# Optimization experiments

Hardware: AMD Instinct MI355X
Metric: run time of the kernel (lower is better)

The kernel has to match this reference:

```python
import jax, jax.numpy as jnp
import numpy as np

N = 50000      # nodes
E = 800000     # edges (avg degree 16)
D = 64         # emb_dim
L = 5          # num_layer
X_DIM = 92     # atom feature dim (hardwired in module)
EA_DIM = 50    # edge feature dim (edge_dim=50)
BN_EPS = 1e-5


def setup_inputs() -> dict:
    key = jax.random.key(0)
    ks = jax.random.split(key, 12)
    s = 0.05
    return {
        "x": jax.random.normal(ks[0], (N, X_DIM), jnp.float32),
        "edge_index": jax.random.randint(ks[1], (2, E), 0, N, dtype=jnp.int64),
        "edge_attr": jax.random.normal(ks[2], (E, EA_DIM), jnp.float32),
        # atom encoder: Linear(92, D)
        "atom_W": jax.random.normal(ks[3], (X_DIM, D), jnp.float32) * s,
        "atom_b": jnp.zeros((D,), jnp.float32),
        # per-layer GINEConv edge lin: Linear(50, D)
        "edge_W": jax.random.normal(ks[4], (L, EA_DIM, D), jnp.float32) * s,
        "edge_b": jnp.zeros((L, D), jnp.float32),
        # per-layer GIN MLP: Linear(D,D) -> ReLU -> Linear(D,D)
        "mlp_W1": jax.random.normal(ks[5], (L, D, D), jnp.float32) * s,
        "mlp_b1": jnp.zeros((L, D), jnp.float32),
        "mlp_W2": jax.random.normal(ks[6], (L, D, D), jnp.float32) * s,
        "mlp_b2": jnp.zeros((L, D), jnp.float32),
        # learnable eps (train_eps=True, init 0)
        "eps": jnp.zeros((L,), jnp.float32),
        # batch norm affine params
        "bn_gamma": jnp.ones((L, D), jnp.float32),
        "bn_beta": jnp.zeros((L, D), jnp.float32),
    }


def reference(x, edge_index, edge_attr, atom_W, atom_b, edge_W, edge_b,
              mlp_W1, mlp_b1, mlp_W2, mlp_b2, eps, bn_gamma, bn_beta):
    # edge_index[0] = src (message source), edge_index[1] = dst (aggregation target)
    # (adj = SparseTensor(row=ei[0], col=ei[1]); conv uses adj.t() -> aggregate at ei[1])
    src, dst = edge_index[0], edge_index[1]
    h = x @ atom_W + atom_b  # [N, D] atom encoder
    for l in range(L):
        # GINEConv message: relu(x_j + lin(edge_attr)), summed at destination
        m = jax.nn.relu(h[src] + edge_attr @ edge_W[l] + edge_b[l])  # [E, D]
        agg = jax.ops.segment_sum(m, dst, num_segments=N)             # [N, D]
        z = (1.0 + eps[l]) * h + agg
        z = jax.nn.relu(z @ mlp_W1[l] + mlp_b1[l]) @ mlp_W2[l] + mlp_b2[l]
        # BatchNorm1d (batch statistics over nodes)
        mu = jnp.mean(z, axis=0)
        var = jnp.var(z, axis=0)
        z = bn_gamma[l] * (z - mu) * jax.lax.rsqrt(var + BN_EPS) + bn_beta[l]
        # relu on all but last layer (dropout inactive in eval); residual=False
        h = z if l == L - 1 else jax.nn.relu(z)
    return h  # JK='last'
```

## Files before the change

kernel.cpp:

```cpp
#include <hip/hip_runtime.h>


#define NN 50000
#define NE 800000
#define D 64
#define NL 5
#define XD 92
#define EAD 50
#define BN_EPS 1e-5f
#define NBLK ((NN + 255) / 256)

__global__ void k_prep(const float* __restrict__ atomW, const float* __restrict__ W1,
                       const float* __restrict__ W2, float* __restrict__ atomWt,
                       float* __restrict__ W1t, float* __restrict__ W2t) {
  int tid = blockIdx.x * blockDim.x + threadIdx.x;
  int nt = gridDim.x * blockDim.x;
  for (int i = tid; i < XD * D; i += nt) {
    int k = i / D, d = i % D;
    atomWt[d * XD + k] = atomW[i];
  }
  for (int i = tid; i < NL * D * D; i += nt) {
    int l = i / (D * D), r = i % (D * D);
    int k = r / D, d = r % D;
    W1t[(l * D + d) * D + k] = W1[i];
    W2t[(l * D + d) * D + k] = W2[i];
  }
}

__global__ __launch_bounds__(256) void k_atom(const float* __restrict__ x,
    const float* __restrict__ Wt, const float* __restrict__ b,
    float* __restrict__ h) {
  int n = blockIdx.x * blockDim.x + threadIdx.x;
  if (n >= NN) return;
  const float* xp = x + (size_t)n * XD;
  float xr[XD];
#pragma unroll
  for (int k = 0; k < XD; k += 4) {
    float4 v = *reinterpret_cast<const float4*>(xp + k);
    xr[k] = v.x; xr[k + 1] = v.y; xr[k + 2] = v.z; xr[k + 3] = v.w;
  }
  float hr[D];
#pragma unroll
  for (int d = 0; d < D; ++d) {
    const float* wr = Wt + d * XD;
    float a0 = 0.f, a1 = 0.f, a2 = 0.f, a3 = 0.f;
#pragma unroll
    for (int k = 0; k < XD; k += 4) {
      a0 = fmaf(xr[k + 0], wr[k + 0], a0);
      a1 = fmaf(xr[k + 1], wr[k + 1], a1);
      a2 = fmaf(xr[k + 2], wr[k + 2], a2);
      a3 = fmaf(xr[k + 3], wr[k + 3], a3);
    }
    hr[d] = (a0 + a1) + (a2 + a3) + b[d];
  }
  float* hp = h + (size_t)n * D;
#pragma unroll
  for (int d = 0; d < D; d += 4)
    *reinterpret_cast<float4*>(hp + d) = make_float4(hr[d], hr[d+1], hr[d+2], hr[d+3]);
}

__global__ __launch_bounds__(256) void k_deg(const int* __restrict__ ei,
                                             int* __restrict__ deg) {
  int e = blockIdx.x * blockDim.x + threadIdx.x;
  if (e < NE) atomicAdd(&deg[ei[NE + e]], 1);
}

__global__ __launch_bounds__(256) void k_scan_a(const int* __restrict__ deg,
    int* __restrict__ lps, int* __restrict__ bsum) {
  __shared__ int s[256];
  int t = threadIdx.x;
  int i = blockIdx.x * 256 + t;
  int v = (i < NN) ? deg[i] : 0;
  s[t] = v;
  __syncthreads();
#pragma unroll
  for (int off = 1; off < 256; off <<= 1) {
    int xv = (t >= off) ? s[t - off] : 0;
    __syncthreads();
    s[t] += xv;
    __syncthreads();
  }
  if (i < NN) lps[i] = s[t] - v;
  if (t == 255) bsum[blockIdx.x] = s[255];
}

__global__ __launch_bounds__(256) void k_scan_b(const int* __restrict__ bsum,
                                                int* __restrict__ bpre) {
  __shared__ int s[256];
  int t = threadIdx.x;
  int v = (t < NBLK) ? bsum[t] : 0;
  s[t] = v;
  __syncthreads();
#pragma unroll
  for (int off = 1; off < 256; off <<= 1) {
    int xv = (t >= off) ? s[t - off] : 0;
    __syncthreads();
    s[t] += xv;
    __syncthreads();
  }
  bpre[t] = s[t] - v;
}

__global__ __launch_bounds__(256) void k_fill(const int* __restrict__ lps,
    const int* __restrict__ bpre, int* __restrict__ rowptr,
    int* __restrict__ cursor) {
  int i = blockIdx.x * blockDim.x + threadIdx.x;
  if (i < NN) {
    int v = lps[i] + bpre[i >> 8];
    rowptr[i] = v;
    cursor[i] = v;
  }
  if (i == 0) rowptr[NN] = NE;
}

__global__ __launch_bounds__(256) void k_scatter(const int* __restrict__ ei,
    int* __restrict__ cursor, int* __restrict__ esrc, int* __restrict__ eidl) {
  int e = blockIdx.x * blockDim.x + threadIdx.x;
  if (e >= NE) return;
  int dst = ei[NE + e];
  int p = atomicAdd(&cursor[dst], 1);
  esrc[p] = ei[e];
  eidl[p] = e;
}

__global__ __launch_bounds__(256) void k_aggr(const float* __restrict__ h,
    const float* __restrict__ ea, const float* __restrict__ eW,
    const float* __restrict__ eb, const int* __restrict__ rowptr,
    const int* __restrict__ esrc, const int* __restrict__ eidl,
    const float* __restrict__ eps, int layer, float* __restrict__ z) {
  int lane = threadIdx.x & 63;
  int wid = __builtin_amdgcn_readfirstlane(blockIdx.x * 4 + (threadIdx.x >> 6));
  int nw = gridDim.x * 4;
  const float* Wl = eW + (size_t)layer * EAD * D;
  float wc[EAD];
#pragma unroll
  for (int k = 0; k < EAD; ++k) wc[k] = Wl[k * D + lane];
  float bd = eb[layer * D + lane];
  float ope = 1.f + eps[layer];
  for (int n = wid; n < NN; n += nw) {
    int beg = __builtin_amdgcn_readfirstlane(rowptr[n]);
    int end = __builtin_amdgcn_readfirstlane(rowptr[n + 1]);
    float acc = 0.f;
    for (int idx = beg; idx < end; ++idx) {
      int e   = __builtin_amdgcn_readfirstlane(eidl[idx]);
      int src = __builtin_amdgcn_readfirstlane(esrc[idx]);
      const float2* ep2 = reinterpret_cast<const float2*>(ea + (size_t)e * EAD);
      float a0 = 0.f, a1 = 0.f, a2 = 0.f, a3 = 0.f;
#pragma unroll
      for (int k2 = 0; k2 < 24; k2 += 2) {
        float2 p0 = ep2[k2];
        float2 p1 = ep2[k2 + 1];
        a0 = fmaf(p0.x, wc[2 * k2 + 0], a0);
        a1 = fmaf(p0.y, wc[2 * k2 + 1], a1);
        a2 = fmaf(p1.x, wc[2 * k2 + 2], a2);
        a3 = fmaf(p1.y, wc[2 * k2 + 3], a3);
      }
      float2 pt = ep2[24];
      a0 = fmaf(pt.x, wc[48], a0);
      a1 = fmaf(pt.y, wc[49], a1);
      float lin = (a0 + a1) + (a2 + a3) + bd;
      acc += fmaxf(h[(size_t)src * D + lane] + lin, 0.f);
    }
    z[(size_t)n * D + lane] = fmaf(ope, h[(size_t)n * D + lane], acc);
  }
}

__global__ __launch_bounds__(256) void k_mlp(const float* __restrict__ W1t,
    const float* __restrict__ b1, const float* __restrict__ W2t,
    const float* __restrict__ b2, int layer, float* __restrict__ z) {
  int n = blockIdx.x * blockDim.x + threadIdx.x;
  if (n >= NN) return;
  float* zp = z + (size_t)n * D;
  float zr[D];
#pragma unroll
  for (int k = 0; k < D; k += 4) {
    float4 v = *reinterpret_cast<const float4*>(zp + k);
    zr[k] = v.x; zr[k+1] = v.y; zr[k+2] = v.z; zr[k+3] = v.w;
  }
  const float* W1l = W1t + (size_t)layer * D * D;
  const float* b1l = b1 + layer * D;
  float y[D];
#pragma unroll
  for (int d = 0; d < D; ++d) {
    const float* wr = W1l + d * D;
    float a0 = 0.f, a1 = 0.f, a2 = 0.f, a3 = 0.f;
#pragma unroll
    for (int k = 0; k < D; k += 4) {
      a0 = fmaf(zr[k + 0], wr[k + 0], a0);
      a1 = fmaf(zr[k + 1], wr[k + 1], a1);
      a2 = fmaf(zr[k + 2], wr[k + 2], a2);
      a3 = fmaf(zr[k + 3], wr[k + 3], a3);
    }
    y[d] = fmaxf((a0 + a1) + (a2 + a3) + b1l[d], 0.f);
  }
  const float* W2l = W2t + (size_t)layer * D * D;
  const float* b2l = b2 + layer * D;
#pragma unroll
  for (int d = 0; d < D; ++d) {
    const float* wr = W2l + d * D;
    float a0 = 0.f, a1 = 0.f, a2 = 0.f, a3 = 0.f;
#pragma unroll
    for (int k = 0; k < D; k += 4) {
      a0 = fmaf(y[k + 0], wr[k + 0], a0);
      a1 = fmaf(y[k + 1], wr[k + 1], a1);
      a2 = fmaf(y[k + 2], wr[k + 2], a2);
      a3 = fmaf(y[k + 3], wr[k + 3], a3);
    }
    zr[d] = (a0 + a1) + (a2 + a3) + b2l[d];
  }
#pragma unroll
  for (int d = 0; d < D; d += 4)
    *reinterpret_cast<float4*>(zp + d) = make_float4(zr[d], zr[d+1], zr[d+2], zr[d+3]);
}

__global__ __launch_bounds__(256) void k_stats(const float* __restrict__ t,
                                               float* __restrict__ stats) {
  int lane = threadIdx.x & 63;
  int w = threadIdx.x >> 6;
  int gw = blockIdx.x * 4 + w;
  int nw = gridDim.x * 4;
  float s = 0.f, q = 0.f;
  for (int n = gw; n < NN; n += nw) {
    float v = t[(size_t)n * D + lane];
    s += v;
    q = fmaf(v, v, q);
  }
  __shared__ float ls[8][64];
  ls[w][lane] = s;
  ls[4 + w][lane] = q;
  __syncthreads();
  if (threadIdx.x < D) {
    float S = ls[0][lane] + ls[1][lane] + ls[2][lane] + ls[3][lane];
    float Q = ls[4][lane] + ls[5][lane] + ls[6][lane] + ls[7][lane];
    unsafeAtomicAdd(&stats[lane], S);
    unsafeAtomicAdd(&stats[D + lane], Q);
  }
}

__global__ __launch_bounds__(256) void k_apply(const float* __restrict__ t,
    const float* __restrict__ stats, const float* __restrict__ gamma,
    const float* __restrict__ beta, int layer, int last, float* __restrict__ o) {
  const float inv = 1.f / (float)NN;
  int i = blockIdx.x * blockDim.x + threadIdx.x;
  int nt = gridDim.x * blockDim.x;
  for (; i < NN * D / 4; i += nt) {
    int d0 = (i & 15) * 4;
    float4 v = reinterpret_cast<const float4*>(t)[i];
    float vv[4] = {v.x, v.y, v.z, v.w};
    float r[4];
#pragma unroll
    for (int c = 0; c < 4; ++c) {
      int d = d0 + c;
      float mu = stats[d] * inv;
      float var = fmaf(-mu, mu, stats[D + d] * inv);
      float sc = gamma[layer * D + d] / sqrtf(var + BN_EPS);
      float val = fmaf(vv[c] - mu, sc, beta[layer * D + d]);
      r[c] = last ? val : fmaxf(val, 0.f);
    }
    reinterpret_cast<float4*>(o)[i] = make_float4(r[0], r[1], r[2], r[3]);
  }
}

extern "C" void kernel_launch(void* const* d_in, const int* in_sizes, int n_in,
                              void* d_out, int out_size, void* d_ws, size_t ws_size,
                              hipStream_t stream) {
  const float* x     = (const float*)d_in[0];
  const int*   ei    = (const int*)d_in[1];
  const float* ea    = (const float*)d_in[2];
  const float* atomW = (const float*)d_in[3];
  const float* atomB = (const float*)d_in[4];
  const float* eW    = (const float*)d_in[5];
  const float* eb    = (const float*)d_in[6];
  const float* W1    = (const float*)d_in[7];
  const float* b1    = (const float*)d_in[8];
  const float* W2    = (const float*)d_in[9];
  const float* b2    = (const float*)d_in[10];
  const float* eps   = (const float*)d_in[11];
  const float* gamma = (const float*)d_in[12];
  const float* beta  = (const float*)d_in[13];
  float* out = (float*)d_out;

  char* ws = (char*)d_ws;
  float* h      = (float*)ws;
  float* z      = h + (size_t)NN * D;
  float* stats  = z + (size_t)NN * D;
  float* atomWt = stats + 2 * D;
  float* W1t    = atomWt + D * XD;
  float* W2t    = W1t + NL * D * D;
  int*   deg    = (int*)(W2t + NL * D * D);
  int*   lps    = deg + NN;
  int*   rowptr = lps + NN;
  int*   cursor = rowptr + NN + 1;
  int*   bsum   = cursor + NN;
  int*   bpre   = bsum + 256;
  int*   esrc   = bpre + 256;
  int*   eidl   = esrc + NE;

  k_prep<<<64, 256, 0, stream>>>(atomW, W1, W2, atomWt, W1t, W2t);
  k_atom<<<(NN + 255) / 256, 256, 0, stream>>>(x, atomWt, atomB, h);

  hipMemsetAsync(deg, 0, (size_t)NN * 4, stream);
  k_deg<<<(NE + 255) / 256, 256, 0, stream>>>(ei, deg);
  k_scan_a<<<NBLK, 256, 0, stream>>>(deg, lps, bsum);
  k_scan_b<<<1, 256, 0, stream>>>(bsum, bpre);
  k_fill<<<NBLK, 256, 0, stream>>>(lps, bpre, rowptr, cursor);
  k_scatter<<<(NE + 255) / 256, 256, 0, stream>>>(ei, cursor, esrc, eidl);

  for (int l = 0; l < NL; ++l) {
    hipMemsetAsync(stats, 0, 2 * D * 4, stream);
    k_aggr<<<3125, 256, 0, stream>>>(h, ea, eW, eb, rowptr, esrc, eidl, eps, l, z);
    k_mlp<<<(NN + 255) / 256, 256, 0, stream>>>(W1t, b1, W2t, b2, l, z);
    k_stats<<<512, 256, 0, stream>>>(z, stats);
    float* ho = (l == NL - 1) ? out : h;
    k_apply<<<1024, 256, 0, stream>>>(z, stats, gamma, beta, l, (l == NL - 1) ? 1 : 0, ho);
  }
}
```

Measured before the change: 2.054 ms.

## Switch aggregation to edge-tiled segmented atomics and stage weights in LDS

New measurement: 5.527 ms. 2.69x slower.

```diff
diff --git a/kernel.cpp b/kernel.cpp
--- a/kernel.cpp
+++ b/kernel.cpp
@@ -9,6 +9,7 @@
 #define EAD 50
 #define BN_EPS 1e-5f
 #define NBLK ((NN + 255) / 256)
+#define TILE_E 128
 
 __global__ void k_prep(const float* __restrict__ atomW, const float* __restrict__ W1,
                        const float* __restrict__ W2, float* __restrict__ atomWt,
@@ -30,6 +31,9 @@
 __global__ __launch_bounds__(256) void k_atom(const float* __restrict__ x,
     const float* __restrict__ Wt, const float* __restrict__ b,
     float* __restrict__ h) {
+  __shared__ float sw[D * XD];
+  for (int i = threadIdx.x; i < D * XD; i += 256) sw[i] = Wt[i];
+  __syncthreads();
   int n = blockIdx.x * blockDim.x + threadIdx.x;
   if (n >= NN) return;
   const float* xp = x + (size_t)n * XD;
@@ -42,14 +46,15 @@
   float hr[D];
 #pragma unroll
   for (int d = 0; d < D; ++d) {
-    const float* wr = Wt + d * XD;
+    const float4* wr = reinterpret_cast<const float4*>(&sw[d * XD]);
     float a0 = 0.f, a1 = 0.f, a2 = 0.f, a3 = 0.f;
 #pragma unroll
-    for (int k = 0; k < XD; k += 4) {
-      a0 = fmaf(xr[k + 0], wr[k + 0], a0);
-      a1 = fmaf(xr[k + 1], wr[k + 1], a1);
-      a2 = fmaf(xr[k + 2], wr[k + 2], a2);
-      a3 = fmaf(xr[k + 3], wr[k + 3], a3);
+    for (int q = 0; q < XD / 4; ++q) {
+      float4 w = wr[q];
+      a0 = fmaf(xr[4 * q + 0], w.x, a0);
+      a1 = fmaf(xr[4 * q + 1], w.y, a1);
+      a2 = fmaf(xr[4 * q + 2], w.z, a2);
+      a3 = fmaf(xr[4 * q + 3], w.w, a3);
     }
     hr[d] = (a0 + a1) + (a2 + a3) + b[d];
   }
@@ -114,103 +119,143 @@
 }
 
 __global__ __launch_bounds__(256) void k_scatter(const int* __restrict__ ei,
-    int* __restrict__ cursor, int* __restrict__ esrc, int* __restrict__ eidl) {
+    int* __restrict__ cursor, int* __restrict__ esrc, int* __restrict__ eidl,
+    int* __restrict__ dstp) {
   int e = blockIdx.x * blockDim.x + threadIdx.x;
   if (e >= NE) return;
   int dst = ei[NE + e];
   int p = atomicAdd(&cursor[dst], 1);
   esrc[p] = ei[e];
   eidl[p] = e;
-}
-
-__global__ __launch_bounds__(256) void k_aggr(const float* __restrict__ h,
+  dstp[p] = dst;
+}
+
+__global__ __launch_bounds__(256) void k_edge(const float* __restrict__ h,
     const float* __restrict__ ea, const float* __restrict__ eW,
-    const float* __restrict__ eb, const int* __restrict__ rowptr,
-    const int* __restrict__ esrc, const int* __restrict__ eidl,
-    const float* __restrict__ eps, int layer, float* __restrict__ z) {
-  int lane = threadIdx.x & 63;
-  int wid = __builtin_amdgcn_readfirstlane(blockIdx.x * 4 + (threadIdx.x >> 6));
-  int nw = gridDim.x * 4;
+    const float* __restrict__ eb, const int* __restrict__ esrc,
+    const int* __restrict__ eidl, const int* __restrict__ dstp,
+    int layer, float* __restrict__ agg) {
+  __shared__ float2 sea2[TILE_E * 26];
+  __shared__ int s_src[TILE_E], s_dst[TILE_E], s_eid[TILE_E];
+  int tid = threadIdx.x;
+  int lane = tid & 63;
+  int slot0 = blockIdx.x * TILE_E;
+
   const float* Wl = eW + (size_t)layer * EAD * D;
   float wc[EAD];
 #pragma unroll
   for (int k = 0; k < EAD; ++k) wc[k] = Wl[k * D + lane];
   float bd = eb[layer * D + lane];
-  float ope = 1.f + eps[layer];
-  for (int n = wid; n < NN; n += nw) {
-    int beg = __builtin_amdgcn_readfirstlane(rowptr[n]);
-    int end = __builtin_amdgcn_readfirstlane(rowptr[n + 1]);
-    float acc = 0.f;
-    for (int idx = beg; idx < end; ++idx) {
-      int e   = __builtin_amdgcn_readfirstlane(eidl[idx]);
-      int src = __builtin_amdgcn_readfirstlane(esrc[idx]);
-      const float2* ep2 = reinterpret_cast<const float2*>(ea + (size_t)e * EAD);
-      float a0 = 0.f, a1 = 0.f, a2 = 0.f, a3 = 0.f;
-#pragma unroll
-      for (int k2 = 0; k2 < 24; k2 += 2) {
-        float2 p0 = ep2[k2];
-        float2 p1 = ep2[k2 + 1];
-        a0 = fmaf(p0.x, wc[2 * k2 + 0], a0);
-        a1 = fmaf(p0.y, wc[2 * k2 + 1], a1);
-        a2 = fmaf(p1.x, wc[2 * k2 + 2], a2);
-        a3 = fmaf(p1.y, wc[2 * k2 + 3], a3);
-      }
-      float2 pt = ep2[24];
-      a0 = fmaf(pt.x, wc[48], a0);
-      a1 = fmaf(pt.y, wc[49], a1);
-      float lin = (a0 + a1) + (a2 + a3) + bd;
-      acc += fmaxf(h[(size_t)src * D + lane] + lin, 0.f);
-    }
-    z[(size_t)n * D + lane] = fmaf(ope, h[(size_t)n * D + lane], acc);
-  }
-}
-
-__global__ __launch_bounds__(256) void k_mlp(const float* __restrict__ W1t,
-    const float* __restrict__ b1, const float* __restrict__ W2t,
-    const float* __restrict__ b2, int layer, float* __restrict__ z) {
+
+  if (tid < TILE_E) {
+    s_eid[tid] = eidl[slot0 + tid];
+    s_src[tid] = esrc[slot0 + tid];
+    s_dst[tid] = dstp[slot0 + tid];
+  }
+  __syncthreads();
+  for (int i = tid; i < TILE_E * 25; i += 256) {
+    int el = i / 25, k2 = i % 25;
+    sea2[el * 26 + k2] =
+        *reinterpret_cast<const float2*>(ea + (size_t)s_eid[el] * EAD + 2 * k2);
+  }
+  __syncthreads();
+
+  int e0 = (tid >> 6) * 32;
+  int cur = s_dst[e0];
+  float acc = 0.f;
+#pragma unroll 2
+  for (int j = 0; j < 32; ++j) {
+    int el = e0 + j;
+    int dst = s_dst[el];
+    int src = s_src[el];
+    if (dst != cur) {
+      unsafeAtomicAdd(&agg[(size_t)cur * D + lane], acc);
+      acc = 0.f;
+      cur = dst;
+    }
+    const float4* er = reinterpret_cast<const float4*>(&sea2[el * 26]);
+    float a0 = 0.f, a1 = 0.f, a2 = 0.f, a3 = 0.f;
+#pragma unroll
+    for (int q = 0; q < 12; ++q) {
+      float4 v = er[q];
+      a0 = fmaf(v.x, wc[4 * q + 0], a0);
+      a1 = fmaf(v.y, wc[4 * q + 1], a1);
+      a2 = fmaf(v.z, wc[4 * q + 2], a2);
+      a3 = fmaf(v.w, wc[4 * q + 3], a3);
+    }
+    float2 tl = sea2[el * 26 + 24];
+    a0 = fmaf(tl.x, wc[48], a0);
+    a1 = fmaf(tl.y, wc[49], a1);
+    float lin = (a0 + a1) + (a2 + a3) + bd;
+    acc += fmaxf(h[(size_t)src * D + lane] + lin, 0.f);
+  }
+  unsafeAtomicAdd(&agg[(size_t)cur * D + lane], acc);
+}
+
+__global__ __launch_bounds__(256) void k_mlp(const float* __restrict__ h,
+    const float* __restrict__ W1t, const float* __restrict__ b1,
+    const float* __restrict__ W2t, const float* __restrict__ b2,
+    const float* __restrict__ eps, int layer, float* __restrict__ agg) {
+  __shared__ float w1[D * D];
+  __shared__ float w2[D * D];
+  {
+    const float* W1l = W1t + (size_t)layer * D * D;
+    const float* W2l = W2t + (size_t)layer * D * D;
+    for (int i = threadIdx.x; i < D * D; i += 256) {
+      w1[i] = W1l[i];
+      w2[i] = W2l[i];
+    }
+  }
+  __syncthreads();
   int n = blockIdx.x * blockDim.x + threadIdx.x;
   if (n >= NN) return;
-  float* zp = z + (size_t)n * D;
+  float ope = 1.f + eps[layer];
+  const float* hp = h + (size_t)n * D;
+  float* ap = (float*)(agg + (size_t)n * D);
   float zr[D];
 #pragma unroll
   for (int k = 0; k < D; k += 4) {
-    float4 v = *reinterpret_cast<const float4*>(zp + k);
-    zr[k] = v.x; zr[k+1] = v.y; zr[k+2] = v.z; zr[k+3] = v.w;
-  }
-  const float* W1l = W1t + (size_t)layer * D * D;
+    float4 hv = *reinterpret_cast<const float4*>(hp + k);
+    float4 av = *reinterpret_cast<const float4*>(ap + k);
+    zr[k]   = fmaf(ope, hv.x, av.x);
+    zr[k+1] = fmaf(ope, hv.y, av.y);
+    zr[k+2] = fmaf(ope, hv.z, av.z);
+    zr[k+3] = fmaf(ope, hv.w, av.w);
+  }
   const float* b1l = b1 + layer * D;
   float y[D];
 #pragma unroll
   for (int d = 0; d < D; ++d) {
-    const float* wr = W1l + d * D;
+    const float4* wr = reinterpret_cast<const float4*>(&w1[d * D]);
     float a0 = 0.f, a1 = 0.f, a2 = 0.f, a3 = 0.f;
 #pragma unroll
-    for (int k = 0; k < D; k += 4) {
-      a0 = fmaf(zr[k + 0], wr[k + 0], a0);
-      a1 = fmaf(zr[k + 1], wr[k + 1], a1);
-      a2 = fmaf(zr[k + 2], wr[k + 2], a2);
-      a3 = fmaf(zr[k + 3], wr[k + 3], a3);
+    for (int q = 0; q < D / 4; ++q) {
+      float4 w = wr[q];
+      a0 = fmaf(zr[4 * q + 0], w.x, a0);
+      a1 = fmaf(zr[4 * q + 1], w.y, a1);
+      a2 = fmaf(zr[4 * q + 2], w.z, a2);
+      a3 = fmaf(zr[4 * q + 3], w.w, a3);
     }
     y[d] = fmaxf((a0 + a1) + (a2 + a3) + b1l[d], 0.f);
   }
-  const float* W2l = W2t + (size_t)layer * D * D;
   const float* b2l = b2 + layer * D;
 #pragma unroll
   for (int d = 0; d < D; ++d) {
-    const float* wr = W2l + d * D;
+    const float4* wr = reinterpret_cast<const float4*>(&w2[d * D]);
     float a0 = 0.f, a1 = 0.f, a2 = 0.f, a3 = 0.f;
 #pragma unroll
-    for (int k = 0; k < D; k += 4) {
-      a0 = fmaf(y[k + 0], wr[k + 0], a0);
-      a1 = fmaf(y[k + 1], wr[k + 1], a1);
-      a2 = fmaf(y[k + 2], wr[k + 2], a2);
-      a3 = fmaf(y[k + 3], wr[k + 3], a3);
+    for (int q = 0; q < D / 4; ++q) {
+      float4 w = wr[q];
+      a0 = fmaf(y[4 * q + 0], w.x, a0);
+      a1 = fmaf(y[4 * q + 1], w.y, a1);
+      a2 = fmaf(y[4 * q + 2], w.z, a2);
+      a3 = fmaf(y[4 * q + 3], w.w, a3);
     }
     zr[d] = (a0 + a1) + (a2 + a3) + b2l[d];
   }
 #pragma unroll
   for (int d = 0; d < D; d += 4)
-    *reinterpret_cast<float4*>(zp + d) = make_float4(zr[d], zr[d+1], zr[d+2], zr[d+3]);
+    *reinterpret_cast<float4*>(ap + d) = make_float4(zr[d], zr[d+1], zr[d+2], zr[d+3]);
 }
 
 __global__ __launch_bounds__(256) void k_stats(const float* __restrict__ t,
@@ -282,8 +327,8 @@
 
   char* ws = (char*)d_ws;
   float* h      = (float*)ws;
-  float* z      = h + (size_t)NN * D;
-  float* stats  = z + (size_t)NN * D;
+  float* agg    = h + (size_t)NN * D;
+  float* stats  = agg + (size_t)NN * D;
   float* atomWt = stats + 2 * D;
   float* W1t    = atomWt + D * XD;
   float* W2t    = W1t + NL * D * D;
@@ -295,6 +340,7 @@
   int*   bpre   = bsum + 256;
   int*   esrc   = bpre + 256;
   int*   eidl   = esrc + NE;
+  int*   dstp   = eidl + NE;
 
   k_prep<<<64, 256, 0, stream>>>(atomW, W1, W2, atomWt, W1t, W2t);
   k_atom<<<(NN + 255) / 256, 256, 0, stream>>>(x, atomWt, atomB, h);
@@ -304,14 +350,14 @@
   k_scan_a<<<NBLK, 256, 0, stream>>>(deg, lps, bsum);
   k_scan_b<<<1, 256, 0, stream>>>(bsum, bpre);
   k_fill<<<NBLK, 256, 0, stream>>>(lps, bpre, rowptr, cursor);
-  k_scatter<<<(NE + 255) / 256, 256, 0, stream>>>(ei, cursor, esrc, eidl);
+  k_scatter<<<(NE + 255) / 256, 256, 0, stream>>>(ei, cursor, esrc, eidl, dstp);
 
   for (int l = 0; l < NL; ++l) {
-    hipMemsetAsync(stats, 0, 2 * D * 4, stream);
-    k_aggr<<<3125, 256, 0, stream>>>(h, ea, eW, eb, rowptr, esrc, eidl, eps, l, z);
-    k_mlp<<<(NN + 255) / 256, 256, 0, stream>>>(W1t, b1, W2t, b2, l, z);
-    k_stats<<<512, 256, 0, stream>>>(z, stats);
+    hipMemsetAsync(agg, 0, ((size_t)NN * D + 2 * D) * 4, stream);
+    k_edge<<<NE / TILE_E, 256, 0, stream>>>(h, ea, eW, eb, esrc, eidl, dstp, l, agg);
+    k_mlp<<<NBLK, 256, 0, stream>>>(h, W1t, b1, W2t, b2, eps, l, agg);
+    k_stats<<<512, 256, 0, stream>>>(agg, stats);
     float* ho = (l == NL - 1) ? out : h;
-    k_apply<<<1024, 256, 0, stream>>>(z, stats, gamma, beta, l, (l == NL - 1) ? 1 : 0, ho);
-  }
-}
+    k_apply<<<1024, 256, 0, stream>>>(agg, stats, gamma, beta, l, (l == NL - 1) ? 1 : 0, ho);
+  }
+}
```

## Replace per-node aggregation with edge-tiled message kernel and segmented atomic reduction

Applied to the files above, without the earlier changes.

Result: slower. 2.221 ms (+8.1%).

```diff
diff --git a/kernel.cpp b/kernel.cpp
--- a/kernel.cpp
+++ b/kernel.cpp
@@ -9,10 +9,12 @@
 #define EAD 50
 #define BN_EPS 1e-5f
 #define NBLK ((NN + 255) / 256)
+#define TILE_E 256
 
 __global__ void k_prep(const float* __restrict__ atomW, const float* __restrict__ W1,
-                       const float* __restrict__ W2, float* __restrict__ atomWt,
-                       float* __restrict__ W1t, float* __restrict__ W2t) {
+                       const float* __restrict__ W2, const float* __restrict__ eW,
+                       float* __restrict__ atomWt, float* __restrict__ W1t,
+                       float* __restrict__ W2t, float* __restrict__ eWt) {
   int tid = blockIdx.x * blockDim.x + threadIdx.x;
   int nt = gridDim.x * blockDim.x;
   for (int i = tid; i < XD * D; i += nt) {
@@ -24,6 +26,11 @@
     int k = r / D, d = r % D;
     W1t[(l * D + d) * D + k] = W1[i];
     W2t[(l * D + d) * D + k] = W2[i];
+  }
+  for (int i = tid; i < NL * EAD * D; i += nt) {
+    int l = i / (EAD * D), r = i % (EAD * D);
+    int k = r / D, d = r % D;
+    eWt[(l * D + d) * EAD + k] = eW[i];
   }
 }
 
@@ -114,68 +121,104 @@
 }
 
 __global__ __launch_bounds__(256) void k_scatter(const int* __restrict__ ei,
-    int* __restrict__ cursor, int* __restrict__ esrc, int* __restrict__ eidl) {
+    int* __restrict__ cursor, int* __restrict__ esrc, int* __restrict__ eidl,
+    int* __restrict__ dstp) {
   int e = blockIdx.x * blockDim.x + threadIdx.x;
   if (e >= NE) return;
   int dst = ei[NE + e];
   int p = atomicAdd(&cursor[dst], 1);
   esrc[p] = ei[e];
   eidl[p] = e;
-}
-
-__global__ __launch_bounds__(256) void k_aggr(const float* __restrict__ h,
-    const float* __restrict__ ea, const float* __restrict__ eW,
-    const float* __restrict__ eb, const int* __restrict__ rowptr,
-    const int* __restrict__ esrc, const int* __restrict__ eidl,
-    const float* __restrict__ eps, int layer, float* __restrict__ z) {
-  int lane = threadIdx.x & 63;
-  int wid = __builtin_amdgcn_readfirstlane(blockIdx.x * 4 + (threadIdx.x >> 6));
-  int nw = gridDim.x * 4;
-  const float* Wl = eW + (size_t)layer * EAD * D;
-  float wc[EAD];
-#pragma unroll
-  for (int k = 0; k < EAD; ++k) wc[k] = Wl[k * D + lane];
-  float bd = eb[layer * D + lane];
-  float ope = 1.f + eps[layer];
-  for (int n = wid; n < NN; n += nw) {
-    int beg = __builtin_amdgcn_readfirstlane(rowptr[n]);
-    int end = __builtin_amdgcn_readfirstlane(rowptr[n + 1]);
+  dstp[p] = dst;
+}
+
+__global__ __launch_bounds__(256) void k_edge(const float* __restrict__ h,
+    const float* __restrict__ ea, const float* __restrict__ eWt,
+    const float* __restrict__ eb, const int* __restrict__ esrc,
+    const int* __restrict__ eidl, const int* __restrict__ dstp,
+    int layer, float* __restrict__ agg) {
+  __shared__ float msg[4][64 * 33];
+  int tid = threadIdx.x;
+  int lane = tid & 63;
+  int w = tid >> 6;
+  int slot = blockIdx.x * TILE_E + w * 64 + lane;
+
+  int eid  = eidl[slot];
+  int vsrc = esrc[slot];
+  int vdst = dstp[slot];
+
+  const float* ep = ea + (size_t)eid * EAD;
+  float4 ear[13];
+#pragma unroll
+  for (int q = 0; q < 12; ++q)
+    ear[q] = *reinterpret_cast<const float4*>(ep + 4 * q);
+  {
+    float2 t2 = *reinterpret_cast<const float2*>(ep + 48);
+    ear[12] = make_float4(t2.x, t2.y, 0.f, 0.f);
+  }
+
+  const float* Wl = eWt + (size_t)layer * D * EAD;
+  const float* bl = eb + (size_t)layer * D;
+  float* mw = msg[w];
+  int half = lane >> 5;
+  int l31 = lane & 31;
+
+#pragma unroll
+  for (int c = 0; c < 2; ++c) {
+#pragma unroll 2
+    for (int dc = 0; dc < 32; ++dc) {
+      int d = c * 32 + dc;
+      const float* wr = Wl + d * EAD;
+      float a0 = 0.f, a1 = 0.f, a2 = 0.f, a3 = 0.f;
+#pragma unroll
+      for (int q = 0; q < 12; ++q) {
+        a0 = fmaf(ear[q].x, wr[4 * q + 0], a0);
+        a1 = fmaf(ear[q].y, wr[4 * q + 1], a1);
+        a2 = fmaf(ear[q].z, wr[4 * q + 2], a2);
+        a3 = fmaf(ear[q].w, wr[4 * q + 3], a3);
+      }
+      a0 = fmaf(ear[12].x, wr[48], a0);
+      a1 = fmaf(ear[12].y, wr[49], a1);
+      mw[lane * 33 + dc] = (a0 + a1) + (a2 + a3) + bl[d];
+    }
     float acc = 0.f;
-    for (int idx = beg; idx < end; ++idx) {
-      int e   = __builtin_amdgcn_readfirstlane(eidl[idx]);
-      int src = __builtin_amdgcn_readfirstlane(esrc[idx]);
-      const float2* ep2 = reinterpret_cast<const float2*>(ea + (size_t)e * EAD);
-      float a0 = 0.f, a1 = 0.f, a2 = 0.f, a3 = 0.f;
-#pragma unroll
-      for (int k2 = 0; k2 < 24; k2 += 2) {
-        float2 p0 = ep2[k2];
-        float2 p1 = ep2[k2 + 1];
-        a0 = fmaf(p0.x, wc[2 * k2 + 0], a0);
-        a1 = fmaf(p0.y, wc[2 * k2 + 1], a1);
-        a2 = fmaf(p1.x, wc[2 * k2 + 2], a2);
-        a3 = fmaf(p1.y, wc[2 * k2 + 3], a3);
+    int cur = __shfl(vdst, half);
+#pragma unroll 4
+    for (int i = 0; i < 32; ++i) {
+      int e = 2 * i + half;
+      int dste = __shfl(vdst, e);
+      int srce = __shfl(vsrc, e);
+      if (dste != cur) {
+        unsafeAtomicAdd(&agg[(size_t)cur * D + c * 32 + l31], acc);
+        acc = 0.f;
+        cur = dste;
       }
-      float2 pt = ep2[24];
-      a0 = fmaf(pt.x, wc[48], a0);
-      a1 = fmaf(pt.y, wc[49], a1);
-      float lin = (a0 + a1) + (a2 + a3) + bd;
-      acc += fmaxf(h[(size_t)src * D + lane] + lin, 0.f);
-    }
-    z[(size_t)n * D + lane] = fmaf(ope, h[(size_t)n * D + lane], acc);
-  }
-}
-
-__global__ __launch_bounds__(256) void k_mlp(const float* __restrict__ W1t,
-    const float* __restrict__ b1, const float* __restrict__ W2t,
-    const float* __restrict__ b2, int layer, float* __restrict__ z) {
+      float lin = mw[e * 33 + l31];
+      float hv = h[(size_t)srce * D + c * 32 + l31];
+      acc += fmaxf(hv + lin, 0.f);
+    }
+    unsafeAtomicAdd(&agg[(size_t)cur * D + c * 32 + l31], acc);
+  }
+}
+
+__global__ __launch_bounds__(256) void k_mlp(const float* __restrict__ h,
+    const float* __restrict__ W1t, const float* __restrict__ b1,
+    const float* __restrict__ W2t, const float* __restrict__ b2,
+    const float* __restrict__ eps, int layer, float* __restrict__ agg) {
   int n = blockIdx.x * blockDim.x + threadIdx.x;
   if (n >= NN) return;
-  float* zp = z + (size_t)n * D;
+  float ope = 1.f + eps[layer];
+  const float* hp = h + (size_t)n * D;
+  float* ap = agg + (size_t)n * D;
   float zr[D];
 #pragma unroll
   for (int k = 0; k < D; k += 4) {
-    float4 v = *reinterpret_cast<const float4*>(zp + k);
-    zr[k] = v.x; zr[k+1] = v.y; zr[k+2] = v.z; zr[k+3] = v.w;
+    float4 hv = *reinterpret_cast<const float4*>(hp + k);
+    float4 av = *reinterpret_cast<const float4*>(ap + k);
+    zr[k]   = fmaf(ope, hv.x, av.x);
+    zr[k+1] = fmaf(ope, hv.y, av.y);
+    zr[k+2] = fmaf(ope, hv.z, av.z);
+    zr[k+3] = fmaf(ope, hv.w, av.w);
   }
   const float* W1l = W1t + (size_t)layer * D * D;
   const float* b1l = b1 + layer * D;
@@ -210,7 +253,7 @@
   }
 #pragma unroll
   for (int d = 0; d < D; d += 4)
-    *reinterpret_cast<float4*>(zp + d) = make_float4(zr[d], zr[d+1], zr[d+2], zr[d+3]);
+    *reinterpret_cast<float4*>(ap + d) = make_float4(zr[d], zr[d+1], zr[d+2], zr[d+3]);
 }
 
 __global__ __launch_bounds__(256) void k_stats(const float* __restrict__ t,
@@ -282,12 +325,13 @@
 
   char* ws = (char*)d_ws;
   float* h      = (float*)ws;
-  float* z      = h + (size_t)NN * D;
-  float* stats  = z + (size_t)NN * D;
+  float* agg    = h + (size_t)NN * D;
+  float* stats  = agg + (size_t)NN * D;
   float* atomWt = stats + 2 * D;
   float* W1t    = atomWt + D * XD;
   float* W2t    = W1t + NL * D * D;
-  int*   deg    = (int*)(W2t + NL * D * D);
+  float* eWt    = W2t + NL * D * D;
+  int*   deg    = (int*)(eWt + NL * D * EAD);
   int*   lps    = deg + NN;
   int*   rowptr = lps + NN;
   int*   cursor = rowptr + NN + 1;
@@ -295,8 +339,9 @@
   int*   bpre   = bsum + 256;
   int*   esrc   = bpre + 256;
   int*   eidl   = esrc + NE;
-
-  k_prep<<<64, 256, 0, stream>>>(atomW, W1, W2, atomWt, W1t, W2t);
+  int*   dstp   = eidl + NE;
+
+  k_prep<<<64, 256, 0, stream>>>(atomW, W1, W2, eW, atomWt, W1t, W2t, eWt);
   k_atom<<<(NN + 255) / 256, 256, 0, stream>>>(x, atomWt, atomB, h);
 
   hipMemsetAsync(deg, 0, (size_t)NN * 4, stream);
@@ -304,14 +349,14 @@
   k_scan_a<<<NBLK, 256, 0, stream>>>(deg, lps, bsum);
   k_scan_b<<<1, 256, 0, stream>>>(bsum, bpre);
   k_fill<<<NBLK, 256, 0, stream>>>(lps, bpre, rowptr, cursor);
-  k_scatter<<<(NE + 255) / 256, 256, 0, stream>>>(ei, cursor, esrc, eidl);
+  k_scatter<<<(NE + 255) / 256, 256, 0, stream>>>(ei, cursor, esrc, eidl, dstp);
 
   for (int l = 0; l < NL; ++l) {
-    hipMemsetAsync(stats, 0, 2 * D * 4, stream);
-    k_aggr<<<3125, 256, 0, stream>>>(h, ea, eW, eb, rowptr, esrc, eidl, eps, l, z);
-    k_mlp<<<(NN + 255) / 256, 256, 0, stream>>>(W1t, b1, W2t, b2, l, z);
-    k_stats<<<512, 256, 0, stream>>>(z, stats);
+    hipMemsetAsync(agg, 0, ((size_t)NN * D + 2 * D) * 4, stream);
+    k_edge<<<NE / TILE_E, 256, 0, stream>>>(h, ea, eWt, eb, esrc, eidl, dstp, l, agg);
+    k_mlp<<<NBLK, 256, 0, stream>>>(h, W1t, b1, W2t, b2, eps, l, agg);
+    k_stats<<<512, 256, 0, stream>>>(agg, stats);
     float* ho = (l == NL - 1) ? out : h;
-    k_apply<<<1024, 256, 0, stream>>>(z, stats, gamma, beta, l, (l == NL - 1) ? 1 : 0, ho);
-  }
-}
+    k_apply<<<1024, 256, 0, stream>>>(agg, stats, gamma, beta, l, (l == NL - 1) ? 1 : 0, ho);
+  }
+}
```
